# Kernel tuning notes

Measured on AMD Instinct MI355X. Metric: run time of the kernel, lower is better.

Reference implementation:

```python
import jax, jax.numpy as jnp
import numpy as np

SEQ, B = 128, 512
PT, EH, ZS, DH, NM, NMAX = 5, 256, 128, 512, 20, 256


def setup_inputs() -> dict:
    key = jax.random.key(0)
    ks = jax.random.split(key, 24)
    rn = lambda k, sh, sc=0.05: jax.random.normal(k, sh, dtype=jnp.float32) * sc
    return {
        "s": rn(ks[0], (SEQ, B, PT), 1.0),
        "enc_Wih_f": rn(ks[1], (4 * EH, PT)), "enc_Whh_f": rn(ks[2], (4 * EH, EH)), "enc_b_f": rn(ks[3], (4 * EH,)),
        "enc_Wih_b": rn(ks[4], (4 * EH, PT)), "enc_Whh_b": rn(ks[5], (4 * EH, EH)), "enc_b_b": rn(ks[6], (4 * EH,)),
        "Wmu": rn(ks[7], (ZS, 2 * EH)), "bmu": rn(ks[8], (ZS,)),
        "Wsig": rn(ks[9], (ZS, 2 * EH)), "bsig": rn(ks[10], (ZS,)),
        "Wh0": rn(ks[11], (DH, ZS)), "bh0": rn(ks[12], (DH,)),
        "dec_Wih": rn(ks[13], (4 * DH, PT + ZS)), "dec_Whh": rn(ks[14], (4 * DH, DH)), "dec_b": rn(ks[15], (4 * DH,)),
        "Wdec": rn(ks[16], (6 * NM + 3, DH)), "bdec": rn(ks[17], (6 * NM + 3,)),
        "z_eps": rn(ks[18], (B, ZS), 1.0),
        "gmm_eps": rn(ks[19], (NMAX, B, NM, 2), 1.0),
        "pen_u": jax.random.uniform(ks[20], (NMAX, B, 3), dtype=jnp.float32),
    }


def _lstm_dir(x, Wih, Whh, b, reverse):
    # PyTorch gate order: i, f, g, o. Returns final hidden state [B, H].
    H = Whh.shape[1]
    Bn = x.shape[1]
    def step(carry, xt):
        h, c = carry
        g = xt @ Wih.T + h @ Whh.T + b
        i, f, gg, o = jnp.split(g, 4, axis=-1)
        c = jax.nn.sigmoid(f) * c + jax.nn.sigmoid(i) * jnp.tanh(gg)
        h = jax.nn.sigmoid(o) * jnp.tanh(c)
        return (h, c), None
    init = (jnp.zeros((Bn, H), x.dtype), jnp.zeros((Bn, H), x.dtype))
    (h, _), _ = jax.lax.scan(step, init, x, reverse=reverse)
    return h


def reference(s, enc_Wih_f, enc_Whh_f, enc_b_f, enc_Wih_b, enc_Whh_b, enc_b_b,
              Wmu, bmu, Wsig, bsig, Wh0, bh0,
              dec_Wih, dec_Whh, dec_b, Wdec, bdec,
              z_eps, gmm_eps, pen_u):
    Bn = s.shape[1]
    # Bidirectional encoder -> concat last hidden states [B, 2*EH]
    hf = _lstm_dir(s, enc_Wih_f, enc_Whh_f, enc_b_f, False)
    hb = _lstm_dir(s, enc_Wih_b, enc_Whh_b, enc_b_b, True)
    h = jnp.concatenate([hf, hb], axis=-1)
    # Reparameterized latent
    mu = h @ Wmu.T + bmu
    sigma = jnp.exp((h @ Wsig.T + bsig) * 0.5)
    z = mu + sigma * z_eps                      # [B, ZS]
    h0 = jnp.tanh(z @ Wh0.T + bh0)              # [B, DH]
    c0 = jnp.zeros_like(h0)
    s0 = jnp.tile(jnp.array([0.0, 0.0, 1.0, 0.0, 0.0], jnp.float32), (Bn, 1))

    def step(carry, noise):
        prev, hc, cc = carry
        eps, u = noise                          # eps [B,NM,2], u [B,3]
        x = jnp.concatenate([prev, z], axis=-1)  # [B, PT+ZS]
        g = x @ dec_Wih.T + hc @ dec_Whh.T + dec_b
        i, f, gg, o = jnp.split(g, 4, axis=-1)
        cc = jax.nn.sigmoid(f) * cc + jax.nn.sigmoid(i) * jnp.tanh(gg)
        hc = jax.nn.sigmoid(o) * jnp.tanh(cc)
        y = hc @ Wdec.T + bdec                  # [B, 6*NM+3]
        mix = y[:, :6 * NM].reshape(Bn, NM, 6)
        pi = jax.nn.softmax(mix[..., 0], axis=-1)
        mx, my = mix[..., 1], mix[..., 2]
        sx, sy = jnp.exp(mix[..., 3]), jnp.exp(mix[..., 4])
        cor = jnp.tanh(mix[..., 5])
        # Sample from N(mean, [[sx^2, cor],[cor, sy^2]]) via Cholesky (cov as in source)
        l21 = cor / sx
        l22 = jnp.sqrt(jnp.maximum(sy * sy - l21 * l21, 1e-6))
        e1, e2 = eps[..., 0], eps[..., 1]
        samp_x = mx + sx * e1
        samp_y = my + l21 * e1 + l22 * e2
        dx = jnp.sum(pi * samp_x, axis=-1)      # pi-weighted sum over mixtures (as in source)
        dy = jnp.sum(pi * samp_y, axis=-1)
        q = jax.nn.softmax(y[:, -3:], axis=-1)
        pen = (u < q).astype(jnp.float32)       # independent Bernoulli thresholds, as in source
        point = jnp.concatenate([dx[:, None], dy[:, None], pen], axis=-1)
        return (point, hc, cc), point

    _, sketch = jax.lax.scan(step, (s0, h0, c0), (gmm_eps, pen_u))
    return sketch  # [NMAX, B, 5]
```

## Files before the change

kernel.cpp:

```cpp
#include <hip/hip_runtime.h>
#include <math.h>

#define B     512
#define SEQL  128
#define PT    5
#define EH    256
#define ZS    128
#define DH    512
#define NM    20
#define NMAXT 256

__device__ __forceinline__ float sigf(float x) { return 1.0f / (1.0f + expf(-x)); }

#define FMA8(m, av, lo, hi)                                                   \
    acc[m][0]=fmaf(av,lo.x,acc[m][0]); acc[m][1]=fmaf(av,lo.y,acc[m][1]);     \
    acc[m][2]=fmaf(av,lo.z,acc[m][2]); acc[m][3]=fmaf(av,lo.w,acc[m][3]);     \
    acc[m][4]=fmaf(av,hi.x,acc[m][4]); acc[m][5]=fmaf(av,hi.y,acc[m][5]);     \
    acc[m][6]=fmaf(av,hi.z,acc[m][6]); acc[m][7]=fmaf(av,hi.w,acc[m][7]);

#define XSUM(v) v += __shfl_xor(v,1); v += __shfl_xor(v,2); v += __shfl_xor(v,4); \
                v += __shfl_xor(v,8); v += __shfl_xor(v,16); v += __shfl_xor(v,32);

__global__ void transpose_pad(const float* __restrict__ in, float* __restrict__ out,
                              int rows, int cols, int rpad, long islice, long oslice)
{
    const float* ip = in + (size_t)blockIdx.z * islice;
    float* op = out + (size_t)blockIdx.z * oslice;
    int idx = blockIdx.x * 256 + threadIdx.x;
    if (idx >= cols * rpad) return;
    int c = idx / rpad, r = idx - c * rpad;
    op[idx] = (r < rows) ? ip[(size_t)r * cols + c] : 0.0f;
}

__global__ __launch_bounds__(512, 4) void enc_step5(
    const float* __restrict__ sT,
    const float* __restrict__ WihF, const float* __restrict__ WhhF, const float* __restrict__ bF,
    const float* __restrict__ WihB, const float* __restrict__ WhhB, const float* __restrict__ bB,
    const float* __restrict__ hfin, float* __restrict__ hfout, float* __restrict__ cf,
    const float* __restrict__ hbin, float* __restrict__ hbout, float* __restrict__ cb,
    int t)
{
    __shared__ float lds[17408];

    const int tid = threadIdx.x;
    const int x   = blockIdx.x;
    const int ng  = x & 31;
    const int bg  = (x >> 5) & 7;
    const int dir = x >> 8;
    const int n0  = ng * 8;
    const int b0  = bg * 64;

    const float* Whh  = dir ? WhhB : WhhF;
    const float* Wih  = dir ? WihB : WihF;
    const float* bias = dir ? bB   : bF;
    const float* hin  = dir ? hbin : hfin;
    float* hout       = dir ? hbout: hfout;
    float* c          = dir ? cb   : cf;
    const int ts = dir ? (SEQL - 1 - t) : t;

    const int pn = tid & 7;
    const int pc = tid >> 3;
    const int pb = b0 + pc;
    const size_t pidx = (size_t)(n0 + pn) * B + pb;
    const float cold = c[pidx];
    const float x0 = sT[((size_t)ts * PT + 0) * B + pb];
    const float x1 = sT[((size_t)ts * PT + 1) * B + pb];
    const float x2 = sT[((size_t)ts * PT + 2) * B + pb];
    const float x3 = sT[((size_t)ts * PT + 3) * B + pb];
    const float x4 = sT[((size_t)ts * PT + 4) * B + pb];

    #pragma unroll
    for (int i = 0; i < 4; ++i) {
        const int fidx = i * 512 + tid;
        const int w   = fidx >> 9;
        const int rem = fidx & 511;
        const int r   = rem >> 4, s5 = rem & 15;
        const int g   = r >> 3, nn = r & 7;
        const float4 wv4 = *(const float4*)&Whh[(size_t)(g * EH + n0 + nn) * EH + w * 64 + s5 * 4];
        *(float4*)&lds[((w * 32 + r) * 16 + (s5 ^ ((r >> 2) & 7))) * 4] = wv4;
    }
    __syncthreads();

    const int lane = tid & 63;
    const int wv   = tid >> 6;
    const int ri   = lane & 7;
    const int bi   = lane >> 3;
    const int wq   = wv >> 1;
    const int sb   = (wv & 1) * 8;
    const float* hcol = hin + b0 + bi * 8;

    float acc[4][8];
    #pragma unroll
    for (int m = 0; m < 4; ++m)
        #pragma unroll
        for (int j = 0; j < 8; ++j) acc[m][j] = 0.0f;

    #pragma unroll 2
    for (int j4 = 0; j4 < 8; ++j4) {
        float4 a[4];
        #pragma unroll
        for (int m = 0; m < 4; ++m)
            a[m] = *(const float4*)&lds[((wq * 32 + ri * 4 + m) * 16 + (sb | (j4 ^ ri))) * 4];
        const int kb = wv * 32 + j4 * 4;
        #pragma unroll
        for (int jj = 0; jj < 4; ++jj) {
            const float* hp = hcol + (size_t)(kb + jj) * B;
            const float4 blo = *(const float4*)hp;
            const float4 bhi = *(const float4*)(hp + 4);
            #pragma unroll
            for (int m = 0; m < 4; ++m) {
                const float av = (jj == 0) ? a[m].x : (jj == 1) ? a[m].y : (jj == 2) ? a[m].z : a[m].w;
                FMA8(m, av, blo, bhi)
            }
        }
    }
    __syncthreads();

    #pragma unroll
    for (int m = 0; m < 4; ++m) {
        float* pr = &lds[(wv * 32 + ri * 4 + m) * 68 + bi * 8];
        *(float4*)pr       = make_float4(acc[m][0], acc[m][1], acc[m][2], acc[m][3]);
        *(float4*)(pr + 4) = make_float4(acc[m][4], acc[m][5], acc[m][6], acc[m][7]);
    }
    __syncthreads();

    float ps[4];
    #pragma unroll
    for (int g = 0; g < 4; ++g) {
        const int r = g * 8 + pn;
        float v = 0.0f;
        #pragma unroll
        for (int w8 = 0; w8 < 8; ++w8) v += lds[(w8 * 32 + r) * 68 + pc];
        ps[g] = v;
    }

    float gv[4];
    #pragma unroll
    for (int g = 0; g < 4; ++g) {
        const int grow = g * EH + n0 + pn;
        const float* wr = Wih + (size_t)grow * PT;
        float v = ps[g] + bias[grow];
        v = fmaf(x0, wr[0], v); v = fmaf(x1, wr[1], v); v = fmaf(x2, wr[2], v);
        v = fmaf(x3, wr[3], v); v = fmaf(x4, wr[4], v);
        gv[g] = v;
    }
    const float cv = sigf(gv[1]) * cold + sigf(gv[0]) * tanhf(gv[2]);
    c[pidx] = cv;
    hout[pidx] = sigf(gv[3]) * tanhf(cv);
}

__global__ __launch_bounds__(512, 4) void dec_step5(
    const float* __restrict__ hin, float* __restrict__ hout, float* __restrict__ cT,
    const float* __restrict__ CzT, const float* __restrict__ Whh,
    const float* __restrict__ Wih, const float* __restrict__ prevPt, int t)
{
    __shared__ float lds[17408];

    const int tid = threadIdx.x;
    const int x   = blockIdx.x;
    const int ng  = x & 63;
    const int bg  = x >> 6;
    const int n0  = ng * 8;
    const int b0  = bg * 64;

    const int pn = tid & 7;
    const int pc = tid >> 3;
    const int pb = b0 + pc;
    const size_t pidx = (size_t)(n0 + pn) * B + pb;
    const float cold = cT[pidx];
    float p0, p1, p2, p3, p4;
    if (t == 0) { p0 = 0.f; p1 = 0.f; p2 = 1.f; p3 = 0.f; p4 = 0.f; }
    else {
        const float* pp = &prevPt[(size_t)pb * 5];
        p0 = pp[0]; p1 = pp[1]; p2 = pp[2]; p3 = pp[3]; p4 = pp[4];
    }
    float cz[4];
    #pragma unroll
    for (int g = 0; g < 4; ++g)
        cz[g] = CzT[(size_t)(g * DH + n0 + pn) * B + pb];

    #pragma unroll
    for (int i = 0; i < 8; ++i) {
        const int fidx = i * 512 + tid;
        const int w   = fidx >> 10;
        const int rem = fidx & 1023;
        const int r   = rem >> 5, s5 = rem & 31;
        const int g   = r >> 3, nn = r & 7;
        const int sl  = (s5 & 16) | ((s5 & 15) ^ ((r >> 2) & 7));
        const float4 wv4 = *(const float4*)&Whh[(size_t)(g * DH + n0 + nn) * DH + w * 128 + s5 * 4];
        *(float4*)&lds[((w * 32 + r) * 32 + sl) * 4] = wv4;
    }
    __syncthreads();

    const int lane = tid & 63;
    const int wv   = tid >> 6;
    const int ri   = lane & 7;
    const int bi   = lane >> 3;
    const int wq   = wv >> 1;
    const int sb   = (wv & 1) * 16;
    const float* hcol = hin + b0 + bi * 8;

    float acc[4][8];
    #pragma unroll
    for (int m = 0; m < 4; ++m)
        #pragma unroll
        for (int j = 0; j < 8; ++j) acc[m][j] = 0.0f;

    #pragma unroll 2
    for (int j4 = 0; j4 < 16; ++j4) {
        float4 a[4];
        #pragma unroll
        for (int m = 0; m < 4; ++m)
            a[m] = *(const float4*)&lds[((wq * 32 + ri * 4 + m) * 32 + (sb | (j4 ^ ri))) * 4];
        const int kb = wv * 64 + j4 * 4;
        #pragma unroll
        for (int jj = 0; jj < 4; ++jj) {
            const float* hp = hcol + (size_t)(kb + jj) * B;
            const float4 blo = *(const float4*)hp;
            const float4 bhi = *(const float4*)(hp + 4);
            #pragma unroll
            for (int m = 0; m < 4; ++m) {
                const float av = (jj == 0) ? a[m].x : (jj == 1) ? a[m].y : (jj == 2) ? a[m].z : a[m].w;
                FMA8(m, av, blo, bhi)
            }
        }
    }
    __syncthreads();

    #pragma unroll
    for (int m = 0; m < 4; ++m) {
        float* pr = &lds[(wv * 32 + ri * 4 + m) * 68 + bi * 8];
        *(float4*)pr       = make_float4(acc[m][0], acc[m][1], acc[m][2], acc[m][3]);
        *(float4*)(pr + 4) = make_float4(acc[m][4], acc[m][5], acc[m][6], acc[m][7]);
    }
    __syncthreads();

    float ps[4];
    #pragma unroll
    for (int g = 0; g < 4; ++g) {
        const int r = g * 8 + pn;
        float v = 0.0f;
        #pragma unroll
        for (int w8 = 0; w8 < 8; ++w8) v += lds[(w8 * 32 + r) * 68 + pc];
        ps[g] = v;
    }

    float gv[4];
    #pragma unroll
    for (int g = 0; g < 4; ++g) {
        const int grow = g * DH + n0 + pn;
        const float* wr = Wih + (size_t)grow * 133;
        float v = ps[g] + cz[g];
        v = fmaf(p0, wr[0], v); v = fmaf(p1, wr[1], v); v = fmaf(p2, wr[2], v);
        v = fmaf(p3, wr[3], v); v = fmaf(p4, wr[4], v);
        gv[g] = v;
    }
    const float cv = sigf(gv[1]) * cold + sigf(gv[0]) * tanhf(gv[2]);
    cT[pidx] = cv;
    hout[pidx] = sigf(gv[3]) * tanhf(cv);
}

__global__ __launch_bounds__(512) void ysamp6(
    const float* __restrict__ hT, const float* __restrict__ WdecT,
    const float* __restrict__ bdec,
    const float* __restrict__ geps, const float* __restrict__ penu,
    float* __restrict__ out, int t)
{
    __shared__ float h_s[512][4];
    __shared__ float part[4][128][4];
    __shared__ float Y[4][128];

    const int tid = threadIdx.x;
    const int col = tid & 127;
    const int ks  = tid >> 7;
    const int b0  = blockIdx.x * 4;

    *(float4*)&h_s[tid][0] = *(const float4*)&hT[(size_t)tid * B + b0];
    __syncthreads();

    float a0 = 0.f, a1 = 0.f, a2 = 0.f, a3 = 0.f;
    const float* wp = WdecT + (size_t)ks * 128 * 128 + col;
    #pragma unroll 8
    for (int k = 0; k < 128; ++k) {
        const float w = wp[(size_t)k * 128];
        const float4 hq = *(const float4*)&h_s[ks * 128 + k][0];
        a0 = fmaf(w, hq.x, a0); a1 = fmaf(w, hq.y, a1);
        a2 = fmaf(w, hq.z, a2); a3 = fmaf(w, hq.w, a3);
    }
    part[ks][col][0] = a0; part[ks][col][1] = a1;
    part[ks][col][2] = a2; part[ks][col][3] = a3;
    __syncthreads();
    if (ks == 0) {
        const float bd = (col < 123) ? bdec[col] : 0.0f;
        #pragma unroll
        for (int j = 0; j < 4; ++j)
            Y[j][col] = part[0][col][j] + part[1][col][j] + part[2][col][j]
                      + part[3][col][j] + bd;
    }
    __syncthreads();

    if (tid < 256) {
        const int bp   = tid >> 6;
        const int lane = tid & 63;
        const int b    = b0 + bp;
        const float* y = Y[bp];
        const int m = lane;
        float pv = (m < NM) ? y[6 * m] : -1e30f;
        float mm = pv;
        mm = fmaxf(mm, __shfl_xor(mm, 1));  mm = fmaxf(mm, __shfl_xor(mm, 2));
        mm = fmaxf(mm, __shfl_xor(mm, 4));  mm = fmaxf(mm, __shfl_xor(mm, 8));
        mm = fmaxf(mm, __shfl_xor(mm, 16)); mm = fmaxf(mm, __shfl_xor(mm, 32));
        float pe = 0.f, tx = 0.f, ty = 0.f;
        if (m < NM) {
            pe = expf(pv - mm);
            const float mx = y[6 * m + 1], my = y[6 * m + 2];
            const float sx = expf(y[6 * m + 3]), sy = expf(y[6 * m + 4]);
            const float cor = tanhf(y[6 * m + 5]);
            const float l21 = cor / sx;
            const float l22 = sqrtf(fmaxf(sy * sy - l21 * l21, 1e-6f));
            const float* ep = &geps[(((size_t)t * B) + b) * (NM * 2) + 2 * m];
            const float e1 = ep[0], e2 = ep[1];
            tx = pe * fmaf(sx, e1, mx);
            ty = pe * (my + fmaf(l21, e1, l22 * e2));
        }
        XSUM(pe) XSUM(tx) XSUM(ty)
        if (lane == 0) {
            const float q0 = y[120], q1 = y[121], q2 = y[122];
            const float qm = fmaxf(q0, fmaxf(q1, q2));
            const float e0 = expf(q0 - qm), e1q = expf(q1 - qm), e2q = expf(q2 - qm);
            const float qs = e0 + e1q + e2q;
            const float* u = &penu[(((size_t)t * B) + b) * 3];
            float* o = &out[(((size_t)t * B) + b) * 5];
            o[0] = tx / pe;
            o[1] = ty / pe;
            o[2] = (u[0] < e0  / qs) ? 1.f : 0.f;
            o[3] = (u[1] < e1q / qs) ? 1.f : 0.f;
            o[4] = (u[2] < e2q / qs) ? 1.f : 0.f;
        }
    }
}

__global__ __launch_bounds__(256) void latent2(
    const float* __restrict__ hfT, const float* __restrict__ hbT,
    const float* __restrict__ Wmu, const float* __restrict__ bmu,
    const float* __restrict__ Wsig, const float* __restrict__ bsig,
    const float* __restrict__ zepsT, float* __restrict__ zT)
{
    const int lane = threadIdx.x & 63;
    const int wv   = __builtin_amdgcn_readfirstlane(threadIdx.x >> 6);
    const int b    = blockIdx.x * 64 + lane;
    const int n0   = blockIdx.y * 8 + wv * 2;

    float am[2] = {}, as2[2] = {};
    #pragma unroll 4
    for (int k0 = 0; k0 < 2 * EH; k0 += 4) {
        const float* hsrc = (k0 < EH) ? hfT : hbT;
        const int kk = k0 & (EH - 1);
        const float a0 = hsrc[(size_t)(kk + 0) * B + b];
        const float a1 = hsrc[(size_t)(kk + 1) * B + b];
        const float a2 = hsrc[(size_t)(kk + 2) * B + b];
        const float a3 = hsrc[(size_t)(kk + 3) * B + b];
        #pragma unroll
        for (int j = 0; j < 2; ++j) {
            const float4 wm = *(const float4*)&Wmu[((size_t)(n0 + j)) * (2 * EH) + k0];
            const float4 ws = *(const float4*)&Wsig[((size_t)(n0 + j)) * (2 * EH) + k0];
            float u = am[j], v = as2[j];
            u = fmaf(a0, wm.x, u); u = fmaf(a1, wm.y, u); u = fmaf(a2, wm.z, u); u = fmaf(a3, wm.w, u);
            v = fmaf(a0, ws.x, v); v = fmaf(a1, ws.y, v); v = fmaf(a2, ws.z, v); v = fmaf(a3, ws.w, v);
            am[j] = u; as2[j] = v;
        }
    }
    #pragma unroll
    for (int j = 0; j < 2; ++j) {
        const int n = n0 + j;
        const float mu = am[j] + bmu[n];
        const float sg = expf(0.5f * (as2[j] + bsig[n]));
        zT[(size_t)n * B + b] = fmaf(sg, zepsT[(size_t)n * B + b], mu);
    }
}

__global__ __launch_bounds__(256) void h02(
    const float* __restrict__ zT, const float* __restrict__ Wh0,
    const float* __restrict__ bh0, float* __restrict__ hT)
{
    const int lane = threadIdx.x & 63;
    const int wv   = __builtin_amdgcn_readfirstlane(threadIdx.x >> 6);
    const int b    = blockIdx.x * 64 + lane;
    const int n0   = blockIdx.y * 32 + wv * 8;

    float acc[8] = {};
    #pragma unroll 2
    for (int k0 = 0; k0 < ZS; k0 += 4) {
        const float a0 = zT[(size_t)(k0 + 0) * B + b];
        const float a1 = zT[(size_t)(k0 + 1) * B + b];
        const float a2 = zT[(size_t)(k0 + 2) * B + b];
        const float a3 = zT[(size_t)(k0 + 3) * B + b];
        #pragma unroll
        for (int r = 0; r < 8; ++r) {
            const float4 w = *(const float4*)&Wh0[((size_t)(n0 + r)) * ZS + k0];
            float v = acc[r];
            v = fmaf(a0, w.x, v); v = fmaf(a1, w.y, v);
            v = fmaf(a2, w.z, v); v = fmaf(a3, w.w, v);
            acc[r] = v;
        }
    }
    #pragma unroll
    for (int r = 0; r < 8; ++r)
        hT[(size_t)(n0 + r) * B + b] = tanhf(acc[r] + bh0[n0 + r]);
}

__global__ __launch_bounds__(256) void cz2(
    const float* __restrict__ zT, const float* __restrict__ Wih,
    const float* __restrict__ bias, float* __restrict__ CzT)
{
    const int lane = threadIdx.x & 63;
    const int wv   = __builtin_amdgcn_readfirstlane(threadIdx.x >> 6);
    const int b    = blockIdx.x * 64 + lane;
    const int r0   = blockIdx.y * 32 + wv * 8;

    float acc[8] = {};
    #pragma unroll 4
    for (int k = 0; k < ZS; ++k) {
        const float a = zT[(size_t)k * B + b];
        #pragma unroll
        for (int r = 0; r < 8; ++r)
            acc[r] = fmaf(a, Wih[(size_t)(r0 + r) * 133 + 5 + k], acc[r]);
    }
    #pragma unroll
    for (int r = 0; r < 8; ++r)
        CzT[(size_t)(r0 + r) * B + b] = acc[r] + bias[r0 + r];
}

extern "C" void kernel_launch(void* const* d_in, const int* in_sizes, int n_in,
                              void* d_out, int out_size, void* d_ws, size_t ws_size,
                              hipStream_t stream)
{
    (void)in_sizes; (void)n_in; (void)out_size; (void)ws_size;

    const float* s      = (const float*)d_in[0];
    const float* WihF   = (const float*)d_in[1];
    const float* WhhF   = (const float*)d_in[2];
    const float* bF     = (const float*)d_in[3];
    const float* WihB   = (const float*)d_in[4];
    const float* WhhB   = (const float*)d_in[5];
    const float* bB     = (const float*)d_in[6];
    const float* Wmu    = (const float*)d_in[7];
    const float* bmu    = (const float*)d_in[8];
    const float* Wsig   = (const float*)d_in[9];
    const float* bsig   = (const float*)d_in[10];
    const float* Wh0    = (const float*)d_in[11];
    const float* bh0    = (const float*)d_in[12];
    const float* decWih = (const float*)d_in[13];
    const float* decWhh = (const float*)d_in[14];
    const float* decB   = (const float*)d_in[15];
    const float* Wdec   = (const float*)d_in[16];
    const float* bdec   = (const float*)d_in[17];
    const float* zeps   = (const float*)d_in[18];
    const float* geps   = (const float*)d_in[19];
    const float* penu   = (const float*)d_in[20];

    float* out = (float*)d_out;
    float* p   = (float*)d_ws;

    float* hf0  = p; p += 131072;
    float* hb0  = p; p += 131072;
    float* cf   = p; p += 131072;
    float* cb   = p; p += 131072;
    float* cdT  = p; p += 262144;
    float* hf1  = p; p += 131072;
    float* hb1  = p; p += 131072;
    float* hA   = p; p += 262144;
    float* hB   = p; p += 262144;
    float* zT   = p; p += 65536;
    float* CzT  = p; p += 1048576;
    float* zepsT= p; p += 65536;
    float* WdecT= p; p += 65536;
    float* sT   = p; p += 327680;

    hipMemsetAsync((void*)hf0, 0, (size_t)(4 * 131072 + 262144) * sizeof(float), stream);

    transpose_pad<<<dim3(256, 1, 1), 256, 0, stream>>>(zeps, zepsT, B, ZS, B, 0, 0);
    transpose_pad<<<dim3(256, 1, 1), 256, 0, stream>>>(Wdec, WdecT, 123, DH, 128, 0, 0);
    transpose_pad<<<dim3(10, 1, SEQL), 256, 0, stream>>>(s, sT, B, PT, B, (long)B * PT, (long)B * PT);

    for (int t = 0; t < SEQL; ++t) {
        const float* hfin = (t & 1) ? hf1 : hf0;  float* hfout = (t & 1) ? hf0 : hf1;
        const float* hbin = (t & 1) ? hb1 : hb0;  float* hbout = (t & 1) ? hb0 : hb1;
        enc_step5<<<dim3(512), 512, 0, stream>>>(
            sT, WihF, WhhF, bF, WihB, WhhB, bB,
            hfin, hfout, cf, hbin, hbout, cb, t);
    }
    latent2<<<dim3(8, 16), 256, 0, stream>>>(hf0, hb0, Wmu, bmu, Wsig, bsig, zepsT, zT);
    h02<<<dim3(8, 16), 256, 0, stream>>>(zT, Wh0, bh0, hA);
    cz2<<<dim3(8, 64), 256, 0, stream>>>(zT, decWih, decB, CzT);

    for (int t = 0; t < NMAXT; ++t) {
        const float* hin = (t & 1) ? hB : hA;
        float* hout      = (t & 1) ? hA : hB;
        dec_step5<<<dim3(512), 512, 0, stream>>>(
            hin, hout, cdT, CzT, decWhh, decWih,
            t ? (out + (size_t)(t - 1) * B * 5) : out, t);
        ysamp6<<<dim3(128), 512, 0, stream>>>(hout, WdecT, bdec, geps, penu, out, t);
    }
}
```

Measured before the change: 9.942 ms.

## Fuse GMM sampling of previous step into decoder step kernel with flag sync

```diff
diff --git a/kernel.cpp b/kernel.cpp
--- a/kernel.cpp
+++ b/kernel.cpp
@@ -20,6 +20,46 @@
 
 #define XSUM(v) v += __shfl_xor(v,1); v += __shfl_xor(v,2); v += __shfl_xor(v,4); \
                 v += __shfl_xor(v,8); v += __shfl_xor(v,16); v += __shfl_xor(v,32);
+
+__device__ __forceinline__ void gmm_sample(
+    const float* __restrict__ y, const float* __restrict__ geps,
+    const float* __restrict__ penu, float* __restrict__ out,
+    int step, int b, int lane)
+{
+    const int m = lane;
+    float pv = (m < NM) ? y[6 * m] : -1e30f;
+    float mm = pv;
+    mm = fmaxf(mm, __shfl_xor(mm, 1));  mm = fmaxf(mm, __shfl_xor(mm, 2));
+    mm = fmaxf(mm, __shfl_xor(mm, 4));  mm = fmaxf(mm, __shfl_xor(mm, 8));
+    mm = fmaxf(mm, __shfl_xor(mm, 16)); mm = fmaxf(mm, __shfl_xor(mm, 32));
+    float pe = 0.f, tx = 0.f, ty = 0.f;
+    if (m < NM) {
+        pe = expf(pv - mm);
+        const float mx = y[6 * m + 1], my = y[6 * m + 2];
+        const float sx = expf(y[6 * m + 3]), sy = expf(y[6 * m + 4]);
+        const float cor = tanhf(y[6 * m + 5]);
+        const float l21 = cor / sx;
+        const float l22 = sqrtf(fmaxf(sy * sy - l21 * l21, 1e-6f));
+        const float* ep = &geps[(((size_t)step * B) + b) * (NM * 2) + 2 * m];
+        const float e1 = ep[0], e2 = ep[1];
+        tx = pe * fmaf(sx, e1, mx);
+        ty = pe * (my + fmaf(l21, e1, l22 * e2));
+    }
+    XSUM(pe) XSUM(tx) XSUM(ty)
+    if (lane == 0) {
+        const float q0 = y[120], q1 = y[121], q2 = y[122];
+        const float qm = fmaxf(q0, fmaxf(q1, q2));
+        const float e0 = expf(q0 - qm), e1q = expf(q1 - qm), e2q = expf(q2 - qm);
+        const float qs = e0 + e1q + e2q;
+        const float* u = &penu[(((size_t)step * B) + b) * 3];
+        float* o = &out[(((size_t)step * B) + b) * 5];
+        o[0] = tx / pe;
+        o[1] = ty / pe;
+        o[2] = (u[0] < e0  / qs) ? 1.f : 0.f;
+        o[3] = (u[1] < e1q / qs) ? 1.f : 0.f;
+        o[4] = (u[2] < e2q / qs) ? 1.f : 0.f;
+    }
+}
 
 __global__ void transpose_pad(const float* __restrict__ in, float* __restrict__ out,
                               int rows, int cols, int rpad, long islice, long oslice)
@@ -149,10 +189,13 @@
     hout[pidx] = sigf(gv[3]) * tanhf(cv);
 }
 
-__global__ __launch_bounds__(512, 4) void dec_step5(
+__global__ __launch_bounds__(512, 4) void dec_fused(
     const float* __restrict__ hin, float* __restrict__ hout, float* __restrict__ cT,
     const float* __restrict__ CzT, const float* __restrict__ Whh,
-    const float* __restrict__ Wih, const float* __restrict__ prevPt, int t)
+    const float* __restrict__ Wih, const float* __restrict__ WdecT,
+    const float* __restrict__ bdec,
+    const float* __restrict__ geps, const float* __restrict__ penu,
+    float* __restrict__ out, int* __restrict__ flags, int t)
 {
     __shared__ float lds[17408];
 
@@ -163,22 +206,58 @@
     const int n0  = ng * 8;
     const int b0  = bg * 64;
 
+    if (t > 0 && ng < 16) {
+        const int tprev = t - 1;
+        const int yb0 = b0 + ng * 4;
+        float* h_s  = lds;
+        float* part = lds + 2048;
+        float* Y    = lds + 4096;
+
+        *(float4*)&h_s[tid * 4] = *(const float4*)&hin[(size_t)tid * B + yb0];
+        __syncthreads();
+
+        const int col = tid & 127;
+        const int ks  = tid >> 7;
+        float a0 = 0.f, a1 = 0.f, a2 = 0.f, a3 = 0.f;
+        const float* wp = WdecT + (size_t)ks * 128 * 128 + col;
+        #pragma unroll 8
+        for (int k = 0; k < 128; ++k) {
+            const float w = wp[(size_t)k * 128];
+            const float4 hq = *(const float4*)&h_s[(ks * 128 + k) * 4];
+            a0 = fmaf(w, hq.x, a0); a1 = fmaf(w, hq.y, a1);
+            a2 = fmaf(w, hq.z, a2); a3 = fmaf(w, hq.w, a3);
+        }
+        float* pc4 = &part[(ks * 128 + col) * 4];
+        pc4[0] = a0; pc4[1] = a1; pc4[2] = a2; pc4[3] = a3;
+        __syncthreads();
+        if (ks == 0) {
+            const float bd = (col < 123) ? bdec[col] : 0.0f;
+            #pragma unroll
+            for (int j = 0; j < 4; ++j)
+                Y[j * 128 + col] = part[(0 * 128 + col) * 4 + j] + part[(128 + col) * 4 + j]
+                                 + part[(256 + col) * 4 + j] + part[(384 + col) * 4 + j] + bd;
+        }
+        __syncthreads();
+        if (tid < 256)
+            gmm_sample(&Y[(tid >> 6) * 128], geps, penu, out, tprev, yb0 + (tid >> 6), tid & 63);
+        __syncthreads();
+        if (tid == 0) {
+            __threadfence();
+            __hip_atomic_fetch_add(&flags[tprev * 8 + bg], 1, __ATOMIC_RELEASE, __HIP_MEMORY_SCOPE_AGENT);
+        }
+    }
+
     const int pn = tid & 7;
     const int pc = tid >> 3;
     const int pb = b0 + pc;
     const size_t pidx = (size_t)(n0 + pn) * B + pb;
     const float cold = cT[pidx];
-    float p0, p1, p2, p3, p4;
-    if (t == 0) { p0 = 0.f; p1 = 0.f; p2 = 1.f; p3 = 0.f; p4 = 0.f; }
-    else {
-        const float* pp = &prevPt[(size_t)pb * 5];
-        p0 = pp[0]; p1 = pp[1]; p2 = pp[2]; p3 = pp[3]; p4 = pp[4];
-    }
     float cz[4];
     #pragma unroll
     for (int g = 0; g < 4; ++g)
         cz[g] = CzT[(size_t)(g * DH + n0 + pn) * B + pb];
 
+    __syncthreads();
     #pragma unroll
     for (int i = 0; i < 8; ++i) {
         const int fidx = i * 512 + tid;
@@ -245,6 +324,18 @@
         ps[g] = v;
     }
 
+    float p0, p1, p2, p3, p4;
+    if (t == 0) { p0 = 0.f; p1 = 0.f; p2 = 1.f; p3 = 0.f; p4 = 0.f; }
+    else {
+        if (tid == 0) {
+            while (__hip_atomic_load(&flags[(t - 1) * 8 + bg], __ATOMIC_ACQUIRE, __HIP_MEMORY_SCOPE_AGENT) < 16)
+                __builtin_amdgcn_s_sleep(1);
+        }
+        __syncthreads();
+        const float* pp = &out[((size_t)(t - 1) * B + pb) * 5];
+        p0 = pp[0]; p1 = pp[1]; p2 = pp[2]; p3 = pp[3]; p4 = pp[4];
+    }
+
     float gv[4];
     #pragma unroll
     for (int g = 0; g < 4; ++g) {
@@ -299,45 +390,8 @@
     }
     __syncthreads();
 
-    if (tid < 256) {
-        const int bp   = tid >> 6;
-        const int lane = tid & 63;
-        const int b    = b0 + bp;
-        const float* y = Y[bp];
-        const int m = lane;
-        float pv = (m < NM) ? y[6 * m] : -1e30f;
-        float mm = pv;
-        mm = fmaxf(mm, __shfl_xor(mm, 1));  mm = fmaxf(mm, __shfl_xor(mm, 2));
-        mm = fmaxf(mm, __shfl_xor(mm, 4));  mm = fmaxf(mm, __shfl_xor(mm, 8));
-        mm = fmaxf(mm, __shfl_xor(mm, 16)); mm = fmaxf(mm, __shfl_xor(mm, 32));
-        float pe = 0.f, tx = 0.f, ty = 0.f;
-        if (m < NM) {
-            pe = expf(pv - mm);
-            const float mx = y[6 * m + 1], my = y[6 * m + 2];
-            const float sx = expf(y[6 * m + 3]), sy = expf(y[6 * m + 4]);
-            const float cor = tanhf(y[6 * m + 5]);
-            const float l21 = cor / sx;
-            const float l22 = sqrtf(fmaxf(sy * sy - l21 * l21, 1e-6f));
-            const float* ep = &geps[(((size_t)t * B) + b) * (NM * 2) + 2 * m];
-            const float e1 = ep[0], e2 = ep[1];
-            tx = pe * fmaf(sx, e1, mx);
-            ty = pe * (my + fmaf(l21, e1, l22 * e2));
-        }
-        XSUM(pe) XSUM(tx) XSUM(ty)
-        if (lane == 0) {
-            const float q0 = y[120], q1 = y[121], q2 = y[122];
-            const float qm = fmaxf(q0, fmaxf(q1, q2));
-            const float e0 = expf(q0 - qm), e1q = expf(q1 - qm), e2q = expf(q2 - qm);
-            const float qs = e0 + e1q + e2q;
-            const float* u = &penu[(((size_t)t * B) + b) * 3];
-            float* o = &out[(((size_t)t * B) + b) * 5];
-            o[0] = tx / pe;
-            o[1] = ty / pe;
-            o[2] = (u[0] < e0  / qs) ? 1.f : 0.f;
-            o[3] = (u[1] < e1q / qs) ? 1.f : 0.f;
-            o[4] = (u[2] < e2q / qs) ? 1.f : 0.f;
-        }
-    }
+    if (tid < 256)
+        gmm_sample(Y[tid >> 6], geps, penu, out, t, b0 + (tid >> 6), tid & 63);
 }
 
 __global__ __launch_bounds__(256) void latent2(
@@ -467,6 +521,7 @@
     float* cf   = p; p += 131072;
     float* cb   = p; p += 131072;
     float* cdT  = p; p += 262144;
+    int*  flags = (int*)p; p += 2048;
     float* hf1  = p; p += 131072;
     float* hb1  = p; p += 131072;
     float* hA   = p; p += 262144;
@@ -477,7 +532,7 @@
     float* WdecT= p; p += 65536;
     float* sT   = p; p += 327680;
 
-    hipMemsetAsync((void*)hf0, 0, (size_t)(4 * 131072 + 262144) * sizeof(float), stream);
+    hipMemsetAsync((void*)hf0, 0, (size_t)(4 * 131072 + 262144 + 2048) * sizeof(float), stream);
 
     transpose_pad<<<dim3(256, 1, 1), 256, 0, stream>>>(zeps, zepsT, B, ZS, B, 0, 0);
     transpose_pad<<<dim3(256, 1, 1), 256, 0, stream>>>(Wdec, WdecT, 123, DH, 128, 0, 0);
@@ -497,9 +552,9 @@
     for (int t = 0; t < NMAXT; ++t) {
         const float* hin = (t & 1) ? hB : hA;
         float* hout      = (t & 1) ? hA : hB;
-        dec_step5<<<dim3(512), 512, 0, stream>>>(
-            hin, hout, cdT, CzT, decWhh, decWih,
-            t ? (out + (size_t)(t - 1) * B * 5) : out, t);
-        ysamp6<<<dim3(128), 512, 0, stream>>>(hout, WdecT, bdec, geps, penu, out, t);
-    }
-}
+        dec_fused<<<dim3(512), 512, 0, stream>>>(
+            hin, hout, cdT, CzT, decWhh, decWih, WdecT, bdec,
+            geps, penu, out, flags, t);
+    }
+    ysamp6<<<dim3(128), 512, 0, stream>>>(hA, WdecT, bdec, geps, penu, out, NMAXT - 1);
+}
```

After: 10.86 ms. 1.09x slower.
